# Performance work log

Hardware: AMD Instinct MI355X
Metric: run time of the kernel (lower is better)

The kernel has to match this reference:

```python
import jax, jax.numpy as jnp
import numpy as np

EPS = 1e-6
WS = 8            # window size
QS = 2            # q_stride


def layernorm(x, g, b):
    m = jnp.mean(x, axis=-1, keepdims=True)
    v = jnp.mean(jnp.square(x - m), axis=-1, keepdims=True)
    return (x - m) * jax.lax.rsqrt(v + EPS) * g + b


def maxpool2x2(x):
    # x: [B,H,W,C] -> [B,H/2,W/2,C]
    B, H, W, C = x.shape
    return x.reshape(B, H // 2, 2, W // 2, 2, C).max(axis=(2, 4))


def window_partition(x, ws):
    B, H, W, C = x.shape
    pad_h = (-H) % ws
    pad_w = (-W) % ws
    x = jnp.pad(x, ((0, 0), (0, pad_h), (0, pad_w), (0, 0)))
    Hp, Wp = H + pad_h, W + pad_w
    x = x.reshape(B, Hp // ws, ws, Wp // ws, ws, C)
    x = x.transpose(0, 1, 3, 2, 4, 5).reshape(-1, ws, ws, C)
    return x, (Hp, Wp)


def window_unpartition(windows, ws, pad_hw, hw):
    Hp, Wp = pad_hw
    H, W = hw
    C = windows.shape[-1]
    B = windows.shape[0] // (Hp * Wp // ws // ws)
    x = windows.reshape(B, Hp // ws, Wp // ws, ws, ws, C)
    x = x.transpose(0, 1, 3, 2, 4, 5).reshape(B, Hp, Wp, C)
    return x[:, :H, :W, :]


def setup_inputs() -> dict:
    key = jax.random.key(0)
    ks = jax.random.split(key, 8)
    B, H, W = 32, 56, 56
    dim, dim_out = 192, 384
    hidden = 4 * dim_out
    s = 0.02
    return {
        "x": jax.random.normal(ks[0], (B, H, W, dim), jnp.float32),
        "norm1_g": jnp.ones((dim,), jnp.float32),
        "norm1_b": jnp.zeros((dim,), jnp.float32),
        "proj_w": jax.random.normal(ks[1], (dim, dim_out), jnp.float32) * s,
        "proj_b": jnp.zeros((dim_out,), jnp.float32),
        "qkv_w": jax.random.normal(ks[2], (dim, 3 * dim_out), jnp.float32) * s,
        "qkv_b": jnp.zeros((3 * dim_out,), jnp.float32),
        "attn_proj_w": jax.random.normal(ks[3], (dim_out, dim_out), jnp.float32) * s,
        "attn_proj_b": jnp.zeros((dim_out,), jnp.float32),
        "norm2_g": jnp.ones((dim_out,), jnp.float32),
        "norm2_b": jnp.zeros((dim_out,), jnp.float32),
        "fc1_w": jax.random.normal(ks[4], (dim_out, hidden), jnp.float32) * s,
        "fc1_b": jnp.zeros((hidden,), jnp.float32),
        "fc2_w": jax.random.normal(ks[5], (hidden, dim_out), jnp.float32) * s,
        "fc2_b": jnp.zeros((dim_out,), jnp.float32),
    }


def reference(x, norm1_g, norm1_b, proj_w, proj_b, qkv_w, qkv_b,
              attn_proj_w, attn_proj_b, norm2_g, norm2_b,
              fc1_w, fc1_b, fc2_w, fc2_b):
    B, H, W, dim = x.shape
    num_heads = 4
    dim_out = attn_proj_w.shape[0]
    head_dim = dim_out // num_heads
    scale = head_dim ** (-0.5)

    xn = layernorm(x, norm1_g, norm1_b)
    # dim != dim_out: shortcut = pooled projection of normed input
    shortcut = maxpool2x2(xn @ proj_w + proj_b)      # [B,H/2,W/2,dim_out]

    # window partition
    w, _ = window_partition(xn, WS)                   # [B*nw, WS, WS, dim]
    Bn = w.shape[0]
    N = WS * WS

    qkv = (w.reshape(Bn, N, dim) @ qkv_w + qkv_b).reshape(Bn, N, 3, num_heads, head_dim)
    q, k, v = qkv[:, :, 0], qkv[:, :, 1], qkv[:, :, 2]

    # q pooling (maxpool 2x2 within each window)
    q = maxpool2x2(q.reshape(Bn, WS, WS, dim_out))    # [Bn, WS/2, WS/2, dim_out]
    wq = WS // QS
    Nq = wq * wq
    q = q.reshape(Bn, Nq, num_heads, head_dim)

    attn = jnp.einsum('bqhd,bkhd->bhqk', q, k) * scale
    attn = jax.nn.softmax(attn, axis=-1)
    out = jnp.einsum('bhqk,bkhd->bqhd', attn, v).reshape(Bn, wq, wq, dim_out)
    out = out @ attn_proj_w + attn_proj_b             # [Bn, wq, wq, dim_out]

    # unpartition at pooled resolution
    Hs, Ws = shortcut.shape[1:3]
    pad_h = (-Hs) % wq
    pad_w = (-Ws) % wq
    out = window_unpartition(out, wq, (Hs + pad_h, Ws + pad_w), (Hs, Ws))

    x = shortcut + out
    h = layernorm(x, norm2_g, norm2_b)
    h = jax.nn.gelu(h @ fc1_w + fc1_b, approximate=False) @ fc2_w + fc2_b
    return x + h
```

## Files before the change

### kernel.cpp

```cpp
#include <hip/hip_runtime.h>
#include <hip/hip_bf16.h>
#include <math.h>

typedef __hip_bfloat16 hbf;
typedef __bf16 bf;
typedef __attribute__((ext_vector_type(8))) __bf16 bf16x8;
typedef __attribute__((ext_vector_type(4))) __bf16 bf16x4;
typedef __attribute__((ext_vector_type(4))) float f32x4;
typedef __attribute__((ext_vector_type(4))) float float4v;

__device__ __forceinline__ float b2f(hbf v) { return __bfloat162float(v); }
__device__ __forceinline__ hbf f2b(float v) { return __float2bfloat16(v); }

#define NP 25088
#define NWIN 1568
#define WSP 396

template <bool BFD>
__device__ __forceinline__ float LD(const void* p, size_t i) {
    if constexpr (BFD) return b2f(((const hbf*)p)[i]);
    else return ((const float*)p)[i];
}
template <bool BFD>
__device__ __forceinline__ void ST(void* p, size_t i, float v) {
    if constexpr (BFD) ((hbf*)p)[i] = f2b(v);
    else ((float*)p)[i] = v;
}
template <bool BFD>
__device__ __forceinline__ void LD8(const void* p, size_t i, float v[8]) {
    if constexpr (BFD) {
        bf16x8 t = *(const bf16x8*)((const hbf*)p + i);
#pragma unroll
        for (int j = 0; j < 8; j++) v[j] = (float)t[j];
    } else {
        float4v a = *(const float4v*)((const float*)p + i);
        float4v c = *(const float4v*)((const float*)p + i + 4);
#pragma unroll
        for (int j = 0; j < 4; j++) { v[j] = a[j]; v[4 + j] = c[j]; }
    }
}
template <bool BFD>
__device__ __forceinline__ void LD4(const void* p, size_t i, float v[4]) {
    if constexpr (BFD) {
        bf16x4 t = *(const bf16x4*)((const hbf*)p + i);
#pragma unroll
        for (int j = 0; j < 4; j++) v[j] = (float)t[j];
    } else {
        float4v a = *(const float4v*)((const float*)p + i);
#pragma unroll
        for (int j = 0; j < 4; j++) v[j] = a[j];
    }
}
template <bool BFD>
__device__ __forceinline__ void ST8(void* p, size_t i, const float v[8]) {
    if constexpr (BFD) {
        bf16x8 t;
#pragma unroll
        for (int j = 0; j < 8; j++) t[j] = (bf)v[j];
        *(bf16x8*)((hbf*)p + i) = t;
    } else {
        float4v a, c;
#pragma unroll
        for (int j = 0; j < 4; j++) { a[j] = v[j]; c[j] = v[4 + j]; }
        *(float4v*)((float*)p + i) = a;
        *(float4v*)((float*)p + i + 4) = c;
    }
}
__device__ __forceinline__ void WS4(bf* w, int idx, const float* v) {
    bf16x4 t;
#pragma unroll
    for (int j = 0; j < 4; j++) t[j] = (bf)v[j];
    *(bf16x4*)(w + idx) = t;
}
__device__ __forceinline__ bool detect_bf16(const void* ones) {
    return *(const unsigned int*)ones == 0x3F803F80u;
}
__device__ __forceinline__ void barls() {
    asm volatile("s_waitcnt lgkmcnt(0)" ::: "memory");
    __builtin_amdgcn_s_barrier();
}

template <bool BFD>
__global__ void __launch_bounds__(768, 3)
attn_window_kernel(const void* __restrict__ x, const void* __restrict__ g,
                   const void* __restrict__ bb, const void* __restrict__ pw,
                   const void* __restrict__ pb, const void* __restrict__ qw,
                   const void* __restrict__ qb, const void* __restrict__ aw,
                   const void* __restrict__ ab, void* __restrict__ x2out) {
    if (detect_bf16(g) != BFD) return;
    __shared__ __align__(16) char smraw[25344 + 2 * 63744];
    bf* ws = (bf*)smraw;
    const int tid = threadIdx.x;
    const int grp = (tid >= 384) ? 1 : 0;
    const int tl  = tid - grp * 384;
    char*  base = smraw + 25344 + grp * 63744;
    bf*    xw   = (bf*)(base);
    bf*    khb  = (bf*)(base + 25600);
    float* pstf = (float*)(base + 25600);
    bf*    vt   = (bf*)(base + 38912);
    bf*    qh   = (bf*)(base + 52736);
    float* Sf   = (float*)(base + 56064);
    bf*    ph   = (bf*)(base + 56064);
    bf*    oh   = (bf*)(base + 60416);
    float* mr   = (float*)(base + 60416);
    float* rr   = (float*)(base + 60672);

    const int wd = blockIdx.x * 2 + grp;
    const int b = wd / 49, rw = wd % 49, wi = rw / 7, wj = rw % 7;
    const int wvl = tl >> 6;
    const int l = tid & 63, lg = l >> 4, lr = l & 15;

    const int sk = tid & 31, sch = tid >> 5;
    auto ld384 = [&](const void* W, int row0, float v[16]) {
        size_t gb = (size_t)(row0 + sk) * 384 + sch * 16;
        LD8<BFD>(W, gb, v);
        LD8<BFD>(W, gb + 8, v + 8);
    };
    auto st384 = [&](const float v[16]) {
        int o = sk * WSP + sch * 16;
#pragma unroll
        for (int i = 0; i < 4; i++) WS4(ws, o + 4 * i, v + 4 * i);
    };
    auto ld288 = [&](int row0, int co, float v[12]) {
        int c0 = sch * 12;
        int gc = co + (c0 % 96) + (c0 / 96) * 384;
        size_t gb = (size_t)(row0 + sk) * 1152 + gc;
#pragma unroll
        for (int i = 0; i < 3; i++) LD4<BFD>(qw, gb + 4 * i, v + 4 * i);
    };
    auto st288 = [&](const float v[12]) {
        int o = sk * WSP + sch * 12;
#pragma unroll
        for (int i = 0; i < 3; i++) WS4(ws, o + 4 * i, v + 4 * i);
    };

#pragma unroll
    for (int rep = 0; rep < 4; rep++) {
        int idx = rep * 3072 + tl * 8;
        int n = idx / 192, cc = idx % 192;
        int h = wi * 8 + (n >> 3), w2 = wj * 8 + (n & 7);
        size_t t = ((size_t)b * 56 + h) * 56 + w2;
        float v[8];
        LD8<BFD>(x, t * 192 + cc, v);
        bf16x8 w8;
#pragma unroll
        for (int j = 0; j < 8; j++) w8[j] = (bf)v[j];
        *(bf16x8*)(xw + n * 200 + cc) = w8;
    }
    barls();
    if (tl < 256) {
        int row = tl >> 2, q = tl & 3;
        float s1 = 0.f, s2 = 0.f;
#pragma unroll
        for (int t = 0; t < 6; t++) {
            bf16x8 v = *(const bf16x8*)(xw + row * 200 + q * 8 + t * 32);
#pragma unroll
            for (int j = 0; j < 8; j++) { float f = (float)v[j]; s1 += f; s2 += f * f; }
        }
        s1 += __shfl_xor(s1, 1, 64); s2 += __shfl_xor(s2, 1, 64);
        s1 += __shfl_xor(s1, 2, 64); s2 += __shfl_xor(s2, 2, 64);
        if (q == 0) {
            float m = s1 / 192.f;
            float var = fmaxf(s2 / 192.f - m * m, 0.f);
            mr[row] = m; rr[row] = rsqrtf(var + 1e-6f);
        }
    }
    barls();
    float sta[16], stb[16];
    float stq[12], stq2[12];
    {
        const int cc0 = (tl % 24) * 8;
        float gv[8], bv[8];
        LD8<BFD>(g, cc0, gv);
        LD8<BFD>(bb, cc0, bv);
#pragma unroll
        for (int rep = 0; rep < 4; rep++) {
            int n = rep * 16 + tl / 24;
            bf16x8 v = *(const bf16x8*)(xw + n * 200 + cc0);
            float m = mr[n], r = rr[n];
            bf16x8 o;
#pragma unroll
            for (int j = 0; j < 8; j++) o[j] = (bf)(((float)v[j] - m) * r * gv[j] + bv[j]);
            *(bf16x8*)(xw + n * 200 + cc0) = o;
        }
    }
    ld384(pw, 0, sta);
    barls();

    {
        f32x4 acc[16];
#pragma unroll
        for (int i = 0; i < 16; i++) acc[i] = (f32x4){0.f, 0.f, 0.f, 0.f};
#pragma unroll
        for (int ks = 0; ks < 6; ks++) {
            if (ks & 1) st384(stb); else st384(sta);
            if (ks < 5) { if (ks & 1) ld384(pw, (ks + 1) * 32, sta); else ld384(pw, (ks + 1) * 32, stb); }
            barls();
#pragma unroll
            for (int ct = 0; ct < 4; ct++) {
                bf16x8 bfr;
#pragma unroll
                for (int j = 0; j < 8; j++)
                    bfr[j] = ws[(lg * 8 + j) * WSP + ct * 96 + wvl * 16 + lr];
#pragma unroll
                for (int m = 0; m < 4; m++) {
                    bf16x8 afr = *(const bf16x8*)(xw + (m * 16 + lr) * 200 + ks * 32 + lg * 8);
                    acc[ct * 4 + m] = __builtin_amdgcn_mfma_f32_16x16x32_bf16(afr, bfr, acc[ct * 4 + m], 0, 0, 0);
                }
            }
            barls();
        }
        ld288(0, 0, stq);
#pragma unroll
        for (int ct = 0; ct < 4; ct++) {
            float pbv = LD<BFD>(pb, ct * 96 + wvl * 16 + lr);
#pragma unroll
            for (int m = 0; m < 4; m++) {
                float v0 = fmaxf(acc[ct * 4 + m][0], acc[ct * 4 + m][1]);
                float v1 = fmaxf(acc[ct * 4 + m][2], acc[ct * 4 + m][3]);
                v0 = fmaxf(v0, __shfl_xor(v0, 32, 64));
                v1 = fmaxf(v1, __shfl_xor(v1, 32, 64));
                if (l < 32) {
                    pstf[(m * 4 + lg * 2 + 0) * 392 + ct * 96 + wvl * 16 + lr] = v0 + pbv;
                    pstf[(m * 4 + lg * 2 + 1) * 392 + ct * 96 + wvl * 16 + lr] = v1 + pbv;
                }
            }
        }
        barls();
        {
            int row = tl / 24, c0 = (tl % 24) * 16;
            int hs = wi * 4 + (row >> 2), wc = wj * 4 + (row & 3);
            size_t gbase = (((size_t)b * 28 + hs) * 28 + wc) * 384 + (size_t)c0;
#pragma unroll
            for (int h8 = 0; h8 < 2; h8++) {
                float v[8];
#pragma unroll
                for (int e = 0; e < 8; e++) v[e] = pstf[row * 392 + c0 + h8 * 8 + e];
                ST8<BFD>(x2out, gbase + h8 * 8, v);
            }
        }
        barls();
    }

    f32x4 pacc[4] = {{0.f,0.f,0.f,0.f},{0.f,0.f,0.f,0.f},{0.f,0.f,0.f,0.f},{0.f,0.f,0.f,0.f}};
    const float scale = 0.1020620726159658f;

    for (int hd = 0; hd < 4; hd++) {
        const int co = hd * 96;
        {
            f32x4 qa[4], ka[4], va[4];
#pragma unroll
            for (int m = 0; m < 4; m++) {
                qa[m] = (f32x4){0.f,0.f,0.f,0.f};
                ka[m] = (f32x4){0.f,0.f,0.f,0.f};
                va[m] = (f32x4){0.f,0.f,0.f,0.f};
            }
#pragma unroll
            for (int ks = 0; ks < 6; ks++) {
                if (ks & 1) st288(stq2); else st288(stq);
                if (ks < 5) { if (ks & 1) ld288((ks + 1) * 32, co, stq); else ld288((ks + 1) * 32, co, stq2); }
                barls();
                bf16x8 bq, bk, bv2;
                const int cl = wvl * 16 + lr;
#pragma unroll
                for (int j = 0; j < 8; j++) {
                    const int ro = (lg * 8 + j) * WSP + cl;
                    bq[j]  = ws[ro];
                    bk[j]  = ws[ro + 96];
                    bv2[j] = ws[ro + 192];
                }
#pragma unroll
                for (int m = 0; m < 4; m++) {
                    bf16x8 afr = *(const bf16x8*)(xw + (m * 16 + lr) * 200 + ks * 32 + lg * 8);
                    qa[m] = __builtin_amdgcn_mfma_f32_16x16x32_bf16(afr, bq,  qa[m], 0, 0, 0);
                    ka[m] = __builtin_amdgcn_mfma_f32_16x16x32_bf16(afr, bk,  ka[m], 0, 0, 0);
                    va[m] = __builtin_amdgcn_mfma_f32_16x16x32_bf16(afr, bv2, va[m], 0, 0, 0);
                }
                barls();
            }
            ld384(aw, co, sta);
            float kbv = LD<BFD>(qb, 384 + co + wvl * 16 + lr);
            float vbv = LD<BFD>(qb, 768 + co + wvl * 16 + lr);
#pragma unroll
            for (int m = 0; m < 4; m++)
#pragma unroll
                for (int r = 0; r < 4; r++) {
                    khb[(m * 16 + lg * 4 + r) * 104 + wvl * 16 + lr] = (bf)(ka[m][r] + kbv);
                    vt[(wvl * 16 + lr) * 72 + m * 16 + lg * 4 + r]   = (bf)(va[m][r] + vbv);
                }
            float qbv = LD<BFD>(qb, co + wvl * 16 + lr);
#pragma unroll
            for (int m = 0; m < 4; m++) {
                float v0 = fmaxf(qa[m][0], qa[m][1]);
                float v1 = fmaxf(qa[m][2], qa[m][3]);
                v0 = fmaxf(v0, __shfl_xor(v0, 32, 64));
                v1 = fmaxf(v1, __shfl_xor(v1, 32, 64));
                if (l < 32) {
                    qh[(m * 4 + lg * 2 + 0) * 104 + wvl * 16 + lr] = (bf)((v0 + qbv) * scale);
                    qh[(m * 4 + lg * 2 + 1) * 104 + wvl * 16 + lr] = (bf)((v1 + qbv) * scale);
                }
            }
        }
        barls();
        if (wvl < 4) {
            f32x4 s = {0.f, 0.f, 0.f, 0.f};
#pragma unroll
            for (int ks = 0; ks < 3; ks++) {
                bf16x8 afr = *(const bf16x8*)(qh + lr * 104 + ks * 32 + lg * 8);
                bf16x8 bfr = *(const bf16x8*)(khb + (wvl * 16 + lr) * 104 + ks * 32 + lg * 8);
                s = __builtin_amdgcn_mfma_f32_16x16x32_bf16(afr, bfr, s, 0, 0, 0);
            }
#pragma unroll
            for (int r = 0; r < 4; r++) Sf[(lg * 4 + r) * 68 + wvl * 16 + lr] = s[r];
        }
        barls();
        if (wvl == 0) {
            int row = l >> 2, q4 = l & 3;
            float e[16];
            float mx = -3.4e38f;
#pragma unroll
            for (int t = 0; t < 16; t++) mx = fmaxf(mx, Sf[row * 68 + q4 * 16 + t]);
            mx = fmaxf(mx, __shfl_xor(mx, 1, 64));
            mx = fmaxf(mx, __shfl_xor(mx, 2, 64));
            float sum = 0.f;
#pragma unroll
            for (int t = 0; t < 16; t++) {
                e[t] = __expf(fminf(fmaxf(Sf[row * 68 + q4 * 16 + t] - mx, -80.f), 0.f));
                sum += e[t];
            }
            sum += __shfl_xor(sum, 1, 64);
            sum += __shfl_xor(sum, 2, 64);
            float inv = 1.f / sum;
#pragma unroll
            for (int t = 0; t < 16; t++) ph[row * 72 + q4 * 16 + t] = (bf)(e[t] * inv);
        }
        barls();
        {
            f32x4 o = {0.f, 0.f, 0.f, 0.f};
#pragma unroll
            for (int ks = 0; ks < 2; ks++) {
                bf16x8 afr = *(const bf16x8*)(ph + lr * 72 + ks * 32 + lg * 8);
                bf16x8 bfr = *(const bf16x8*)(vt + (wvl * 16 + lr) * 72 + ks * 32 + lg * 8);
                o = __builtin_amdgcn_mfma_f32_16x16x32_bf16(afr, bfr, o, 0, 0, 0);
            }
#pragma unroll
            for (int r = 0; r < 4; r++) oh[(lg * 4 + r) * 104 + wvl * 16 + lr] = (bf)o[r];
        }
        barls();
#pragma unroll
        for (int ks2 = 0; ks2 < 3; ks2++) {
            if (ks2 & 1) st384(stb); else st384(sta);
            if (ks2 < 2) { if (ks2 & 1) ld384(aw, co + (ks2 + 1) * 32, sta); else ld384(aw, co + (ks2 + 1) * 32, stb); }
            if (ks2 == 1 && hd < 3) ld288(0, co + 96, stq);
            barls();
            bf16x8 afr = *(const bf16x8*)(oh + lr * 104 + ks2 * 32 + lg * 8);
#pragma unroll
            for (int t = 0; t < 4; t++) {
                bf16x8 bfr;
#pragma unroll
                for (int j = 0; j < 8; j++)
                    bfr[j] = ws[(lg * 8 + j) * WSP + wvl * 64 + t * 16 + lr];
                pacc[t] = __builtin_amdgcn_mfma_f32_16x16x32_bf16(afr, bfr, pacc[t], 0, 0, 0);
            }
            barls();
        }
    }

#pragma unroll
    for (int t = 0; t < 4; t++) {
        int c = wvl * 64 + t * 16 + lr;
        float abv = LD<BFD>(ab, c);
#pragma unroll
        for (int r = 0; r < 4; r++)
            pstf[(lg * 4 + r) * 392 + c] = pacc[t][r] + abv;
    }
    barls();
    {
        int row = tl / 24, c0 = (tl % 24) * 16;
        int hs = wi * 4 + (row >> 2), wc = wj * 4 + (row & 3);
        size_t gbase = (((size_t)b * 28 + hs) * 28 + wc) * 384 + (size_t)c0;
#pragma unroll
        for (int h8 = 0; h8 < 2; h8++) {
            float v[8];
            LD8<BFD>(x2out, gbase + h8 * 8, v);
#pragma unroll
            for (int e = 0; e < 8; e++) v[e] += pstf[row * 392 + c0 + h8 * 8 + e];
            ST8<BFD>(x2out, gbase + h8 * 8, v);
        }
    }
}

template <bool BFD>
__global__ void __launch_bounds__(512, 3)
mlp_kernel(const void* __restrict__ flagp, const void* __restrict__ n2g,
           const void* __restrict__ n2b, const void* __restrict__ w1,
           const void* __restrict__ b1, const void* __restrict__ w2,
           const void* __restrict__ b2p, void* __restrict__ outp) {
    if (detect_bf16(flagp) != BFD) return;
    __shared__ __align__(16) bf xin[64 * 392];
    __shared__ __align__(16) bf hch[64 * 136];
    __shared__ float mr2[64], rr2[64];
    const size_t r0 = (size_t)blockIdx.x * 64;
    const int tid = threadIdx.x;
    const int wv = tid >> 6, l = tid & 63, lg = l >> 4, lr = l & 15;

    for (int i = tid; i < 64 * 384; i += 512) {
        int n = i / 384, c = i % 384;
        xin[n * 392 + c] = (bf)LD<BFD>(outp, (r0 + n) * 384 + c);
    }
    __syncthreads();
    if (tid < 64) {
        float s1 = 0.f, s2 = 0.f;
        for (int k = 0; k < 384; k += 8) {
            bf16x8 v = *(const bf16x8*)(xin + tid * 392 + k);
#pragma unroll
            for (int j = 0; j < 8; j++) { float f = (float)v[j]; s1 += f; s2 += f * f; }
        }
        float m = s1 / 384.f;
        float var = fmaxf(s2 / 384.f - m * m, 0.f);
        mr2[tid] = m; rr2[tid] = rsqrtf(var + 1e-6f);
    }
    __syncthreads();
    for (int i = tid; i < 64 * 384; i += 512) {
        int n = i / 384, c = i % 384;
        xin[n * 392 + c] = (bf)(((float)xin[n * 392 + c] - mr2[n]) * rr2[n] * LD<BFD>(n2g, c) + LD<BFD>(n2b, c));
    }
    __syncthreads();

    f32x4 pacc[12];
#pragma unroll
    for (int i = 0; i < 12; i++) pacc[i] = (f32x4){0.f, 0.f, 0.f, 0.f};

    for (int kb = 0; kb < 12; kb++) {
        f32x4 hacc[4] = {{0.f,0.f,0.f,0.f},{0.f,0.f,0.f,0.f},{0.f,0.f,0.f,0.f},{0.f,0.f,0.f,0.f}};
        const int c1 = kb * 128 + wv * 16 + lr;
        for (int ks = 0; ks < 12; ks++) {
            bf16x8 bfr;
#pragma unroll
            for (int j = 0; j < 8; j++)
                bfr[j] = (bf)LD<BFD>(w1, (size_t)(ks * 32 + lg * 8 + j) * 1536 + (size_t)c1);
#pragma unroll
            for (int m = 0; m < 4; m++) {
                bf16x8 afr = *(const bf16x8*)(xin + (m * 16 + lr) * 392 + ks * 32 + lg * 8);
                hacc[m] = __builtin_amdgcn_mfma_f32_16x16x32_bf16(afr, bfr, hacc[m], 0, 0, 0);
            }
        }
        float bv = LD<BFD>(b1, c1);
        __syncthreads();
#pragma unroll
        for (int m = 0; m < 4; m++)
#pragma unroll
            for (int r = 0; r < 4; r++) {
                float hv = hacc[m][r] + bv;
                hv = 0.5f * hv * (1.f + erff(hv * 0.70710678118f));
                hch[(m * 16 + lg * 4 + r) * 136 + wv * 16 + lr] = (bf)hv;
            }
        __syncthreads();
        for (int ks = 0; ks < 4; ks++) {
#pragma unroll
            for (int t = 0; t < 3; t++) {
                int c = wv * 48 + t * 16 + lr;
                bf16x8 bfr;
#pragma unroll
                for (int j = 0; j < 8; j++)
                    bfr[j] = (bf)LD<BFD>(w2, (size_t)(kb * 128 + ks * 32 + lg * 8 + j) * 384 + (size_t)c);
#pragma unroll
                for (int m = 0; m < 4; m++) {
                    bf16x8 afr = *(const bf16x8*)(hch + (m * 16 + lr) * 136 + ks * 32 + lg * 8);
                    pacc[m * 3 + t] = __builtin_amdgcn_mfma_f32_16x16x32_bf16(afr, bfr, pacc[m * 3 + t], 0, 0, 0);
                }
            }
        }
    }

#pragma unroll
    for (int t = 0; t < 3; t++) {
        int c = wv * 48 + t * 16 + lr;
        float bv = LD<BFD>(b2p, c);
#pragma unroll
        for (int m = 0; m < 4; m++)
#pragma unroll
            for (int r = 0; r < 4; r++) {
                size_t idx = (r0 + (size_t)(m * 16 + lg * 4 + r)) * 384 + (size_t)c;
                ST<BFD>(outp, idx, LD<BFD>(outp, idx) + pacc[m * 3 + t][r] + bv);
            }
    }
}

extern "C" void kernel_launch(void* const* d_in, const int* in_sizes, int n_in,
                              void* d_out, int out_size, void* d_ws, size_t ws_size,
                              hipStream_t stream) {
    const void* x    = d_in[0];
    const void* n1g  = d_in[1];
    const void* n1b  = d_in[2];
    const void* pw   = d_in[3];
    const void* pb   = d_in[4];
    const void* qw   = d_in[5];
    const void* qb   = d_in[6];
    const void* aw   = d_in[7];
    const void* ab   = d_in[8];
    const void* n2g  = d_in[9];
    const void* n2b  = d_in[10];
    const void* f1w  = d_in[11];
    const void* f1b  = d_in[12];
    const void* f2w  = d_in[13];
    const void* f2b_ = d_in[14];

    attn_window_kernel<true ><<<NWIN / 2, 768, 0, stream>>>(x, n1g, n1b, pw, pb, qw, qb, aw, ab, d_out);
    attn_window_kernel<false><<<NWIN / 2, 768, 0, stream>>>(x, n1g, n1b, pw, pb, qw, qb, aw, ab, d_out);
    mlp_kernel<true ><<<NP / 64, 512, 0, stream>>>(n1g, n2g, n2b, f1w, f1b, f2w, f2b_, d_out);
    mlp_kernel<false><<<NP / 64, 512, 0, stream>>>(n1g, n2g, n2b, f1w, f1b, f2w, f2b_, d_out);
}
```

Baseline: 710.1 us.

## Stage weights transposed in LDS for vector B-fragment reads; stage MLP weights through LDS

Weight tiles are now written to shared memory in a k-contiguous transposed layout, so MFMA B fragments load as one 16-byte read instead of eight scalar strided LDS reads. The global weight loads become column-wise coalesced scalar loads across threads. The MLP kernel, which previously gathered fc1/fc2 weights per lane straight from global memory, now double-buffers them through an LDS tile with barriers, and its column mapping for fc2 is reorganized. Occupancy hint for the MLP kernel is raised. The cost is extra barriers per k-step and more shared memory.

New measurement: 600.9 us. 1.18x faster.

```diff
diff --git a/kernel.cpp b/kernel.cpp
--- a/kernel.cpp
+++ b/kernel.cpp
@@ -14,7 +14,7 @@
 
 #define NP 25088
 #define NWIN 1568
-#define WSP 396
+#define TKS 40
 
 template <bool BFD>
 __device__ __forceinline__ float LD(const void* p, size_t i) {
@@ -40,18 +40,6 @@
     }
 }
 template <bool BFD>
-__device__ __forceinline__ void LD4(const void* p, size_t i, float v[4]) {
-    if constexpr (BFD) {
-        bf16x4 t = *(const bf16x4*)((const hbf*)p + i);
-#pragma unroll
-        for (int j = 0; j < 4; j++) v[j] = (float)t[j];
-    } else {
-        float4v a = *(const float4v*)((const float*)p + i);
-#pragma unroll
-        for (int j = 0; j < 4; j++) v[j] = a[j];
-    }
-}
-template <bool BFD>
 __device__ __forceinline__ void ST8(void* p, size_t i, const float v[8]) {
     if constexpr (BFD) {
         bf16x8 t;
@@ -66,11 +54,11 @@
         *(float4v*)((float*)p + i + 4) = c;
     }
 }
-__device__ __forceinline__ void WS4(bf* w, int idx, const float* v) {
-    bf16x4 t;
-#pragma unroll
-    for (int j = 0; j < 4; j++) t[j] = (bf)v[j];
-    *(bf16x4*)(w + idx) = t;
+__device__ __forceinline__ void WPK8(bf* w, int idx, const float* v) {
+    bf16x8 t;
+#pragma unroll
+    for (int j = 0; j < 8; j++) t[j] = (bf)v[j];
+    *(bf16x8*)(w + idx) = t;
 }
 __device__ __forceinline__ bool detect_bf16(const void* ones) {
     return *(const unsigned int*)ones == 0x3F803F80u;
@@ -88,12 +76,12 @@
                    const void* __restrict__ qb, const void* __restrict__ aw,
                    const void* __restrict__ ab, void* __restrict__ x2out) {
     if (detect_bf16(g) != BFD) return;
-    __shared__ __align__(16) char smraw[25344 + 2 * 63744];
-    bf* ws = (bf*)smraw;
+    __shared__ __align__(16) char smraw[30720 + 2 * 63744];
+    bf* wsT = (bf*)smraw;
     const int tid = threadIdx.x;
     const int grp = (tid >= 384) ? 1 : 0;
     const int tl  = tid - grp * 384;
-    char*  base = smraw + 25344 + grp * 63744;
+    char*  base = smraw + 30720 + grp * 63744;
     bf*    xw   = (bf*)(base);
     bf*    khb  = (bf*)(base + 25600);
     float* pstf = (float*)(base + 25600);
@@ -110,28 +98,30 @@
     const int wvl = tl >> 6;
     const int l = tid & 63, lg = l >> 4, lr = l & 15;
 
-    const int sk = tid & 31, sch = tid >> 5;
+    const int sc384 = tid % 384, sr384 = (tid / 384) * 16;
+    const int sc288 = tid % 288, sr288 = (tid / 288) * 16;
     auto ld384 = [&](const void* W, int row0, float v[16]) {
-        size_t gb = (size_t)(row0 + sk) * 384 + sch * 16;
-        LD8<BFD>(W, gb, v);
-        LD8<BFD>(W, gb + 8, v + 8);
+#pragma unroll
+        for (int i = 0; i < 16; i++)
+            v[i] = LD<BFD>(W, (size_t)(row0 + sr384 + i) * 384 + sc384);
     };
     auto st384 = [&](const float v[16]) {
-        int o = sk * WSP + sch * 16;
-#pragma unroll
-        for (int i = 0; i < 4; i++) WS4(ws, o + 4 * i, v + 4 * i);
+        WPK8(wsT, sc384 * TKS + sr384, v);
+        WPK8(wsT, sc384 * TKS + sr384 + 8, v + 8);
     };
-    auto ld288 = [&](int row0, int co, float v[12]) {
-        int c0 = sch * 12;
-        int gc = co + (c0 % 96) + (c0 / 96) * 384;
-        size_t gb = (size_t)(row0 + sk) * 1152 + gc;
-#pragma unroll
-        for (int i = 0; i < 3; i++) LD4<BFD>(qw, gb + 4 * i, v + 4 * i);
+    auto ld288 = [&](int row0, int co, float v[16]) {
+        if (tid < 576) {
+            int gc = co + (sc288 % 96) + (sc288 / 96) * 384;
+#pragma unroll
+            for (int i = 0; i < 16; i++)
+                v[i] = LD<BFD>(qw, (size_t)(row0 + sr288 + i) * 1152 + gc);
+        }
     };
-    auto st288 = [&](const float v[12]) {
-        int o = sk * WSP + sch * 12;
-#pragma unroll
-        for (int i = 0; i < 3; i++) WS4(ws, o + 4 * i, v + 4 * i);
+    auto st288 = [&](const float v[16]) {
+        if (tid < 576) {
+            WPK8(wsT, sc288 * TKS + sr288, v);
+            WPK8(wsT, sc288 * TKS + sr288 + 8, v + 8);
+        }
     };
 
 #pragma unroll
@@ -167,7 +157,7 @@
     }
     barls();
     float sta[16], stb[16];
-    float stq[12], stq2[12];
+    float stq[16], stq2[16];
     {
         const int cc0 = (tl % 24) * 8;
         float gv[8], bv[8];
@@ -198,10 +188,7 @@
             barls();
 #pragma unroll
             for (int ct = 0; ct < 4; ct++) {
-                bf16x8 bfr;
-#pragma unroll
-                for (int j = 0; j < 8; j++)
-                    bfr[j] = ws[(lg * 8 + j) * WSP + ct * 96 + wvl * 16 + lr];
+                bf16x8 bfr = *(const bf16x8*)(wsT + (ct * 96 + wvl * 16 + lr) * TKS + lg * 8);
 #pragma unroll
                 for (int m = 0; m < 4; m++) {
                     bf16x8 afr = *(const bf16x8*)(xw + (m * 16 + lr) * 200 + ks * 32 + lg * 8);
@@ -255,20 +242,15 @@
                 ka[m] = (f32x4){0.f,0.f,0.f,0.f};
                 va[m] = (f32x4){0.f,0.f,0.f,0.f};
             }
+            const int cl = wvl * 16 + lr;
 #pragma unroll
             for (int ks = 0; ks < 6; ks++) {
                 if (ks & 1) st288(stq2); else st288(stq);
                 if (ks < 5) { if (ks & 1) ld288((ks + 1) * 32, co, stq); else ld288((ks + 1) * 32, co, stq2); }
                 barls();
-                bf16x8 bq, bk, bv2;
-                const int cl = wvl * 16 + lr;
-#pragma unroll
-                for (int j = 0; j < 8; j++) {
-                    const int ro = (lg * 8 + j) * WSP + cl;
-                    bq[j]  = ws[ro];
-                    bk[j]  = ws[ro + 96];
-                    bv2[j] = ws[ro + 192];
-                }
+                bf16x8 bq  = *(const bf16x8*)(wsT + cl * TKS + lg * 8);
+                bf16x8 bk  = *(const bf16x8*)(wsT + (96 + cl) * TKS + lg * 8);
+                bf16x8 bv2 = *(const bf16x8*)(wsT + (192 + cl) * TKS + lg * 8);
 #pragma unroll
                 for (int m = 0; m < 4; m++) {
                     bf16x8 afr = *(const bf16x8*)(xw + (m * 16 + lr) * 200 + ks * 32 + lg * 8);
@@ -356,10 +338,7 @@
             bf16x8 afr = *(const bf16x8*)(oh + lr * 104 + ks2 * 32 + lg * 8);
 #pragma unroll
             for (int t = 0; t < 4; t++) {
-                bf16x8 bfr;
-#pragma unroll
-                for (int j = 0; j < 8; j++)
-                    bfr[j] = ws[(lg * 8 + j) * WSP + wvl * 64 + t * 16 + lr];
+                bf16x8 bfr = *(const bf16x8*)(wsT + (wvl * 64 + t * 16 + lr) * TKS + lg * 8);
                 pacc[t] = __builtin_amdgcn_mfma_f32_16x16x32_bf16(afr, bfr, pacc[t], 0, 0, 0);
             }
             barls();
@@ -391,7 +370,7 @@
 }
 
 template <bool BFD>
-__global__ void __launch_bounds__(512, 3)
+__global__ void __launch_bounds__(512, 4)
 mlp_kernel(const void* __restrict__ flagp, const void* __restrict__ n2g,
            const void* __restrict__ n2b, const void* __restrict__ w1,
            const void* __restrict__ b1, const void* __restrict__ w2,
@@ -399,16 +378,25 @@
     if (detect_bf16(flagp) != BFD) return;
     __shared__ __align__(16) bf xin[64 * 392];
     __shared__ __align__(16) bf hch[64 * 136];
+    __shared__ __align__(16) bf wsT[128 * TKS];
     __shared__ float mr2[64], rr2[64];
     const size_t r0 = (size_t)blockIdx.x * 64;
     const int tid = threadIdx.x;
     const int wv = tid >> 6, l = tid & 63, lg = l >> 4, lr = l & 15;
 
+    const int mc = tid & 127, mrw = (tid >> 7) * 8;
+    auto ldw = [&](const void* W, int ldN, int row0, int col0, float v[8]) {
+#pragma unroll
+        for (int i = 0; i < 8; i++)
+            v[i] = LD<BFD>(W, (size_t)(row0 + mrw + i) * ldN + col0 + mc);
+    };
+    auto stw = [&](const float v[8]) { WPK8(wsT, mc * TKS + mrw, v); };
+
     for (int i = tid; i < 64 * 384; i += 512) {
         int n = i / 384, c = i % 384;
         xin[n * 392 + c] = (bf)LD<BFD>(outp, (r0 + n) * 384 + c);
     }
-    __syncthreads();
+    barls();
     if (tid < 64) {
         float s1 = 0.f, s2 = 0.f;
         for (int k = 0; k < 384; k += 8) {
@@ -420,69 +408,78 @@
         float var = fmaxf(s2 / 384.f - m * m, 0.f);
         mr2[tid] = m; rr2[tid] = rsqrtf(var + 1e-6f);
     }
-    __syncthreads();
+    barls();
     for (int i = tid; i < 64 * 384; i += 512) {
         int n = i / 384, c = i % 384;
         xin[n * 392 + c] = (bf)(((float)xin[n * 392 + c] - mr2[n]) * rr2[n] * LD<BFD>(n2g, c) + LD<BFD>(n2b, c));
     }
-    __syncthreads();
+    barls();
 
     f32x4 pacc[12];
 #pragma unroll
     for (int i = 0; i < 12; i++) pacc[i] = (f32x4){0.f, 0.f, 0.f, 0.f};
+    float wA[8], wB[8];
+    const int cl = wv * 16 + lr;
 
     for (int kb = 0; kb < 12; kb++) {
         f32x4 hacc[4] = {{0.f,0.f,0.f,0.f},{0.f,0.f,0.f,0.f},{0.f,0.f,0.f,0.f},{0.f,0.f,0.f,0.f}};
-        const int c1 = kb * 128 + wv * 16 + lr;
+        ldw(w1, 1536, 0, kb * 128, wA);
+#pragma unroll
         for (int ks = 0; ks < 12; ks++) {
-            bf16x8 bfr;
-#pragma unroll
-            for (int j = 0; j < 8; j++)
-                bfr[j] = (bf)LD<BFD>(w1, (size_t)(ks * 32 + lg * 8 + j) * 1536 + (size_t)c1);
+            if (ks & 1) stw(wB); else stw(wA);
+            if (ks < 11) { if (ks & 1) ldw(w1, 1536, (ks + 1) * 32, kb * 128, wA); else ldw(w1, 1536, (ks + 1) * 32, kb * 128, wB); }
+            barls();
+            bf16x8 bfr = *(const bf16x8*)(wsT + cl * TKS + lg * 8);
 #pragma unroll
             for (int m = 0; m < 4; m++) {
                 bf16x8 afr = *(const bf16x8*)(xin + (m * 16 + lr) * 392 + ks * 32 + lg * 8);
                 hacc[m] = __builtin_amdgcn_mfma_f32_16x16x32_bf16(afr, bfr, hacc[m], 0, 0, 0);
             }
-        }
-        float bv = LD<BFD>(b1, c1);
-        __syncthreads();
-#pragma unroll
-        for (int m = 0; m < 4; m++)
-#pragma unroll
-            for (int r = 0; r < 4; r++) {
-                float hv = hacc[m][r] + bv;
-                hv = 0.5f * hv * (1.f + erff(hv * 0.70710678118f));
-                hch[(m * 16 + lg * 4 + r) * 136 + wv * 16 + lr] = (bf)hv;
-            }
-        __syncthreads();
-        for (int ks = 0; ks < 4; ks++) {
-#pragma unroll
-            for (int t = 0; t < 3; t++) {
-                int c = wv * 48 + t * 16 + lr;
-                bf16x8 bfr;
-#pragma unroll
-                for (int j = 0; j < 8; j++)
-                    bfr[j] = (bf)LD<BFD>(w2, (size_t)(kb * 128 + ks * 32 + lg * 8 + j) * 384 + (size_t)c);
-#pragma unroll
-                for (int m = 0; m < 4; m++) {
-                    bf16x8 afr = *(const bf16x8*)(hch + (m * 16 + lr) * 136 + ks * 32 + lg * 8);
-                    pacc[m * 3 + t] = __builtin_amdgcn_mfma_f32_16x16x32_bf16(afr, bfr, pacc[m * 3 + t], 0, 0, 0);
+            barls();
+        }
+        ldw(w2, 384, kb * 128, 0, wA);
+        {
+            float bv = LD<BFD>(b1, kb * 128 + cl);
+#pragma unroll
+            for (int m = 0; m < 4; m++)
+#pragma unroll
+                for (int r = 0; r < 4; r++) {
+                    float hv = hacc[m][r] + bv;
+                    hv = 0.5f * hv * (1.f + erff(hv * 0.70710678118f));
+                    hch[(m * 16 + lg * 4 + r) * 136 + cl] = (bf)hv;
                 }
-            }
-        }
-    }
-
-#pragma unroll
-    for (int t = 0; t < 3; t++) {
-        int c = wv * 48 + t * 16 + lr;
+        }
+        barls();
+#pragma unroll
+        for (int p = 0; p < 12; p++) {
+            const int cb = p >> 2, ks = p & 3;
+            if (p & 1) stw(wB); else stw(wA);
+            if (p < 11) {
+                const int pn = p + 1;
+                if (p & 1) ldw(w2, 384, kb * 128 + (pn & 3) * 32, (pn >> 2) * 128, wA);
+                else       ldw(w2, 384, kb * 128 + (pn & 3) * 32, (pn >> 2) * 128, wB);
+            }
+            barls();
+            bf16x8 bfr = *(const bf16x8*)(wsT + cl * TKS + lg * 8);
+#pragma unroll
+            for (int m = 0; m < 4; m++) {
+                bf16x8 afr = *(const bf16x8*)(hch + (m * 16 + lr) * 136 + ks * 32 + lg * 8);
+                pacc[cb * 4 + m] = __builtin_amdgcn_mfma_f32_16x16x32_bf16(afr, bfr, pacc[cb * 4 + m], 0, 0, 0);
+            }
+            barls();
+        }
+    }
+
+#pragma unroll
+    for (int cb = 0; cb < 3; cb++) {
+        int c = cb * 128 + cl;
         float bv = LD<BFD>(b2p, c);
 #pragma unroll
         for (int m = 0; m < 4; m++)
 #pragma unroll
             for (int r = 0; r < 4; r++) {
                 size_t idx = (r0 + (size_t)(m * 16 + lg * 4 + r)) * 384 + (size_t)c;
-                ST<BFD>(outp, idx, LD<BFD>(outp, idx) + pacc[m * 3 + t][r] + bv);
+                ST<BFD>(outp, idx, LD<BFD>(outp, idx) + pacc[cb * 4 + m][r] + bv);
             }
     }
 }
```
